# Kernel optimization log

Hardware: AMD Instinct MI355X
Metric: run time of the kernel (lower is better)

## Reference

```python
import jax, jax.numpy as jnp
import numpy as np

# ---- config constants (TwoCompartmentLIFConfig defaults) ----
DT = 1.0                      # ms per Euler step
G_L, E_L = 0.05, 0.0          # somatic leak
G_L_D = 0.03                  # dendritic leak
C_D = 0.5                     # dendritic capacitance
G_C = 0.05                    # soma-dendrite coupling
E_E, E_I = 3.0, -0.5
E_NMDA, E_GABA_B = 3.0, -0.8
E_CA = 4.0
E_ADAPT = -0.5
V_TH, V_RESET, TAU_REF = 1.0, 0.0, 5.0
MG_K, MG_VHALF = 5.0, 0.5     # NMDA Mg2+ block sigmoid
THETA_CA, G_CA_SPIKE = 2.0, 0.3
BAP_AMP = 0.3
ADAPT_INC = 0.0
# conductance decay factors exp(-dt/tau)
D_E  = float(np.exp(-DT / 5.0))
D_I  = float(np.exp(-DT / 10.0))
D_N  = float(np.exp(-DT / 100.0))
D_GB = float(np.exp(-DT / 400.0))
D_CA = float(np.exp(-DT / 20.0))
D_AD = float(np.exp(-DT / 100.0))

T, N = 50, 500000
IN_SCALE = 0.06


def setup_inputs() -> dict:
    key = jax.random.key(0)
    ks = jax.random.split(key, 7)
    names = ["g_exc_basal", "g_inh_basal", "g_nmda_basal", "g_gaba_b_in",
             "g_exc_apical", "g_inh_apical", "g_nmda_apical"]
    return {n: IN_SCALE * jax.random.uniform(k, (T, N), dtype=jnp.float32)
            for n, k in zip(names, ks)}


def _run(g_exc_basal, g_inh_basal, g_nmda_basal, g_gaba_b_in,
         g_exc_apical, g_inh_apical, g_nmda_apical):
    n = g_exc_basal.shape[1]
    z = jnp.zeros((n,), jnp.float32)
    # carry: v_soma, v_dend, gEb, gIb, gNb, gGB, gEa, gIa, gNa, gCa, gAd, ref
    carry0 = (z + E_L, z + E_L, z, z, z, z, z, z, z, z, z, z)

    def step(carry, inp):
        v_s, v_d, gEb, gIb, gNb, gGB, gEa, gIa, gNa, gCa, gAd, ref = carry
        in_Eb, in_Ib, in_Nb, in_GB, in_Ea, in_Ia, in_Na = inp
        # decay + inject synaptic conductances
        gEb = gEb * D_E + in_Eb
        gIb = gIb * D_I + in_Ib
        gNb = gNb * D_N + in_Nb
        gGB = gGB * D_GB + in_GB
        gEa = gEa * D_E + in_Ea
        gIa = gIa * D_I + in_Ia
        gNa = gNa * D_N + in_Na
        gCa = gCa * D_CA
        # NMDA Mg2+ block gated at the LOCAL compartment voltage
        mg_s = jax.nn.sigmoid(MG_K * (v_s - MG_VHALF))
        mg_d = jax.nn.sigmoid(MG_K * (v_d - MG_VHALF))
        # somatic current (C_m = 1)
        I_s = (G_L * (E_L - v_s) + gEb * (E_E - v_s) + gIb * (E_I - v_s)
               + gNb * mg_s * (E_NMDA - v_s) + gGB * (E_GABA_B - v_s)
               + gAd * (E_ADAPT - v_s) + G_C * (v_d - v_s))
        # dendritic current
        I_d = (G_L_D * (E_L - v_d) + gEa * (E_E - v_d) + gIa * (E_I - v_d)
               + gNa * mg_d * (E_NMDA - v_d) + gCa * (E_CA - v_d)
               + G_C * (v_s - v_d))
        refractory = ref > 0.0
        v_s = jnp.where(refractory, V_RESET, v_s + DT * I_s)
        v_d = v_d + (DT / C_D) * I_d
        # spike + reset + refractory
        spike = (v_s >= V_TH) & jnp.logical_not(refractory)
        spike_f = spike.astype(jnp.float32)
        v_s = jnp.where(spike, V_RESET, v_s)
        ref = jnp.where(spike, TAU_REF, jnp.maximum(ref - DT, 0.0))
        gAd = gAd * D_AD + spike_f * ADAPT_INC
        # back-propagating AP depolarises dendrite
        v_d = jnp.where(spike, v_d + BAP_AMP * (E_CA - v_d), v_d)
        # dendritic Ca spike
        gCa = gCa + (v_d >= THETA_CA).astype(jnp.float32) * G_CA_SPIKE
        carry = (v_s, v_d, gEb, gIb, gNb, gGB, gEa, gIa, gNa, gCa, gAd, ref)
        return carry, (spike_f, v_s)

    inputs = (g_exc_basal, g_inh_basal, g_nmda_basal, g_gaba_b_in,
              g_exc_apical, g_inh_apical, g_nmda_apical)
    _, (spikes, v_trace) = jax.lax.scan(step, carry0, inputs)
    return spikes, v_trace  # each [T, N]


def reference(g_exc_basal, g_inh_basal, g_nmda_basal, g_gaba_b_in,
              g_exc_apical, g_inh_apical, g_nmda_apical):
    return _run(g_exc_basal, g_inh_basal, g_nmda_basal, g_gaba_b_in,
                g_exc_apical, g_inh_apical, g_nmda_apical)
```

## Files before the change

kernel.cpp:

```cpp
#include <hip/hip_runtime.h>
#include <math.h>

namespace {
constexpr float D_E   = 0.8187307530779818f;
constexpr float D_I   = 0.9048374180359595f;
constexpr float D_N   = 0.9900498337491681f;
constexpr float D_GB  = 0.9975031223974601f;
constexpr float D_CA  = 0.9512294245007140f;

constexpr float DT      = 1.0f;
constexpr float G_L     = 0.05f;
constexpr float E_L     = 0.0f;
constexpr float G_L_D   = 0.03f;
constexpr float DT_C_D  = 2.0f;
constexpr float G_C     = 0.05f;
constexpr float E_E     = 3.0f;
constexpr float E_I     = -0.5f;
constexpr float E_NMDA  = 3.0f;
constexpr float E_GABA_B= -0.8f;
constexpr float E_CA    = 4.0f;
constexpr float V_TH    = 1.0f;
constexpr float V_RESET = 0.0f;
constexpr float TAU_REF = 5.0f;
constexpr float MG_K    = 5.0f;
constexpr float MG_VHALF= 0.5f;
constexpr float THETA_CA= 2.0f;
constexpr float G_CA_SPIKE = 0.3f;
constexpr float BAP_AMP = 0.3f;
}

__device__ __forceinline__ void lif_step(
    float in_Eb, float in_Ib, float in_Nb, float in_GB,
    float in_Ea, float in_Ia, float in_Na,
    float& v_s, float& v_d,
    float& gEb, float& gIb, float& gNb, float& gGB,
    float& gEa, float& gIa, float& gNa, float& gCa, float& ref,
    float& spike_out, float& v_out)
{
    gEb = gEb * D_E  + in_Eb;
    gIb = gIb * D_I  + in_Ib;
    gNb = gNb * D_N  + in_Nb;
    gGB = gGB * D_GB + in_GB;
    gEa = gEa * D_E  + in_Ea;
    gIa = gIa * D_I  + in_Ia;
    gNa = gNa * D_N  + in_Na;
    gCa = gCa * D_CA;

    const float mg_s = 1.0f / (1.0f + expf(-MG_K * (v_s - MG_VHALF)));
    const float mg_d = 1.0f / (1.0f + expf(-MG_K * (v_d - MG_VHALF)));

    const float I_s = G_L * (E_L - v_s) + gEb * (E_E - v_s) + gIb * (E_I - v_s)
                    + gNb * mg_s * (E_NMDA - v_s) + gGB * (E_GABA_B - v_s)
                    + G_C * (v_d - v_s);
    const float I_d = G_L_D * (E_L - v_d) + gEa * (E_E - v_d) + gIa * (E_I - v_d)
                    + gNa * mg_d * (E_NMDA - v_d) + gCa * (E_CA - v_d)
                    + G_C * (v_s - v_d);

    const bool refractory = ref > 0.0f;
    v_s = refractory ? V_RESET : (v_s + DT * I_s);
    v_d = v_d + DT_C_D * I_d;

    const bool spike = (v_s >= V_TH) && !refractory;
    const float spike_f = spike ? 1.0f : 0.0f;
    v_s = spike ? V_RESET : v_s;
    ref = spike ? TAU_REF : fmaxf(ref - DT, 0.0f);
    v_d = spike ? (v_d + BAP_AMP * (E_CA - v_d)) : v_d;
    gCa = gCa + ((v_d >= THETA_CA) ? G_CA_SPIKE : 0.0f);

    spike_out = spike_f;
    v_out = v_s;
}

__global__ __launch_bounds__(256, 8)
void lif_scalar_pf_kernel(const float* __restrict__ pEb, const float* __restrict__ pIb,
                          const float* __restrict__ pNb, const float* __restrict__ pGB,
                          const float* __restrict__ pEa, const float* __restrict__ pIa,
                          const float* __restrict__ pNa,
                          float* __restrict__ out, int N, int T)
{
    const int i = blockIdx.x * blockDim.x + threadIdx.x;
    if (i >= N) return;

    float v_s = E_L, v_d = E_L;
    float gEb = 0, gIb = 0, gNb = 0, gGB = 0;
    float gEa = 0, gIa = 0, gNa = 0, gCa = 0, ref = 0;

    const size_t vtrace_off = (size_t)T * (size_t)N;

    size_t off = (size_t)i;
    float nEb = pEb[off], nIb = pIb[off], nNb = pNb[off], nGB = pGB[off];
    float nEa = pEa[off], nIa = pIa[off], nNa = pNa[off];

    for (int t = 0; t < T; ++t) {
        const float cEb = nEb, cIb = nIb, cNb = nNb, cGB = nGB;
        const float cEa = nEa, cIa = nIa, cNa = nNa;

        const size_t noff = off + ((t + 1 < T) ? (size_t)N : 0);
        nEb = pEb[noff]; nIb = pIb[noff]; nNb = pNb[noff]; nGB = pGB[noff];
        nEa = pEa[noff]; nIa = pIa[noff]; nNa = pNa[noff];

        float sp, vv;
        lif_step(cEb, cIb, cNb, cGB, cEa, cIa, cNa,
                 v_s, v_d, gEb, gIb, gNb, gGB, gEa, gIa, gNa, gCa, ref,
                 sp, vv);

        out[off]              = sp;
        out[vtrace_off + off] = vv;
        off += (size_t)N;
    }
}

extern "C" void kernel_launch(void* const* d_in, const int* in_sizes, int n_in,
                              void* d_out, int out_size, void* d_ws, size_t ws_size,
                              hipStream_t stream) {
    const float* pEb = (const float*)d_in[0];
    const float* pIb = (const float*)d_in[1];
    const float* pNb = (const float*)d_in[2];
    const float* pGB = (const float*)d_in[3];
    const float* pEa = (const float*)d_in[4];
    const float* pIa = (const float*)d_in[5];
    const float* pNa = (const float*)d_in[6];
    float* out = (float*)d_out;

    const int T = 50;
    const int N = in_sizes[0] / T;

    const int blocks = (N + 255) / 256;
    lif_scalar_pf_kernel<<<blocks, 256, 0, stream>>>(pEb, pIb, pNb, pGB, pEa, pIa, pNa,
                                                     out, N, T);
}
```

Baseline: 180.8 us.

## Process two neurons per thread with float2 loads, two-step prefetch, nontemporal stores

Each thread now handles two adjacent neurons and uses 8-byte vector loads and stores. It keeps two timesteps of inputs in flight as a double-buffered prefetch and writes outputs with nontemporal stores. The sigmoid is switched to fast exp and divide intrinsics, and launch bounds drop to 4 blocks per SM. The goal is more memory-level parallelism and fewer memory instructions in a bandwidth-bound scan, at the cost of more registers, half as many threads, and a small loss of precision in the sigmoid.

```diff
diff --git a/kernel.cpp b/kernel.cpp
--- a/kernel.cpp
+++ b/kernel.cpp
@@ -29,84 +29,151 @@
 constexpr float BAP_AMP = 0.3f;
 }
 
-__device__ __forceinline__ void lif_step(
-    float in_Eb, float in_Ib, float in_Nb, float in_GB,
-    float in_Ea, float in_Ia, float in_Na,
-    float& v_s, float& v_d,
-    float& gEb, float& gIb, float& gNb, float& gGB,
-    float& gEa, float& gIa, float& gNa, float& gCa, float& ref,
-    float& spike_out, float& v_out)
-{
-    gEb = gEb * D_E  + in_Eb;
-    gIb = gIb * D_I  + in_Ib;
-    gNb = gNb * D_N  + in_Nb;
-    gGB = gGB * D_GB + in_GB;
-    gEa = gEa * D_E  + in_Ea;
-    gIa = gIa * D_I  + in_Ia;
-    gNa = gNa * D_N  + in_Na;
-    gCa = gCa * D_CA;
-
-    const float mg_s = 1.0f / (1.0f + expf(-MG_K * (v_s - MG_VHALF)));
-    const float mg_d = 1.0f / (1.0f + expf(-MG_K * (v_d - MG_VHALF)));
-
-    const float I_s = G_L * (E_L - v_s) + gEb * (E_E - v_s) + gIb * (E_I - v_s)
-                    + gNb * mg_s * (E_NMDA - v_s) + gGB * (E_GABA_B - v_s)
-                    + G_C * (v_d - v_s);
-    const float I_d = G_L_D * (E_L - v_d) + gEa * (E_E - v_d) + gIa * (E_I - v_d)
-                    + gNa * mg_d * (E_NMDA - v_d) + gCa * (E_CA - v_d)
-                    + G_C * (v_s - v_d);
-
-    const bool refractory = ref > 0.0f;
-    v_s = refractory ? V_RESET : (v_s + DT * I_s);
-    v_d = v_d + DT_C_D * I_d;
-
-    const bool spike = (v_s >= V_TH) && !refractory;
-    const float spike_f = spike ? 1.0f : 0.0f;
-    v_s = spike ? V_RESET : v_s;
-    ref = spike ? TAU_REF : fmaxf(ref - DT, 0.0f);
-    v_d = spike ? (v_d + BAP_AMP * (E_CA - v_d)) : v_d;
-    gCa = gCa + ((v_d >= THETA_CA) ? G_CA_SPIKE : 0.0f);
-
-    spike_out = spike_f;
-    v_out = v_s;
+typedef float f32x2 __attribute__((ext_vector_type(2)));
+
+__device__ __forceinline__ float fast_sigmoid5(float v) {
+    return __fdividef(1.0f, 1.0f + __expf(-MG_K * (v - MG_VHALF)));
+}
+
+struct State2 {
+    float v_s[2], v_d[2];
+    float gEb[2], gIb[2], gNb[2], gGB[2];
+    float gEa[2], gIa[2], gNa[2], gCa[2], ref[2];
+};
+
+__device__ __forceinline__ void absorb2(
+    const f32x2 iEb, const f32x2 iIb, const f32x2 iNb, const f32x2 iGB,
+    const f32x2 iEa, const f32x2 iIa, const f32x2 iNa, State2& s)
+{
+    s.gEb[0] = s.gEb[0]*D_E  + iEb.x;  s.gEb[1] = s.gEb[1]*D_E  + iEb.y;
+    s.gIb[0] = s.gIb[0]*D_I  + iIb.x;  s.gIb[1] = s.gIb[1]*D_I  + iIb.y;
+    s.gNb[0] = s.gNb[0]*D_N  + iNb.x;  s.gNb[1] = s.gNb[1]*D_N  + iNb.y;
+    s.gGB[0] = s.gGB[0]*D_GB + iGB.x;  s.gGB[1] = s.gGB[1]*D_GB + iGB.y;
+    s.gEa[0] = s.gEa[0]*D_E  + iEa.x;  s.gEa[1] = s.gEa[1]*D_E  + iEa.y;
+    s.gIa[0] = s.gIa[0]*D_I  + iIa.x;  s.gIa[1] = s.gIa[1]*D_I  + iIa.y;
+    s.gNa[0] = s.gNa[0]*D_N  + iNa.x;  s.gNa[1] = s.gNa[1]*D_N  + iNa.y;
+    s.gCa[0] *= D_CA;                  s.gCa[1] *= D_CA;
+}
+
+__device__ __forceinline__ void fire2(State2& s, f32x2& osp, f32x2& ov)
+{
+    #pragma unroll
+    for (int j = 0; j < 2; ++j) {
+        float v_s = s.v_s[j], v_d = s.v_d[j];
+        const float mg_s = fast_sigmoid5(v_s);
+        const float mg_d = fast_sigmoid5(v_d);
+        const float I_s = G_L*(E_L - v_s) + s.gEb[j]*(E_E - v_s) + s.gIb[j]*(E_I - v_s)
+                        + s.gNb[j]*mg_s*(E_NMDA - v_s) + s.gGB[j]*(E_GABA_B - v_s)
+                        + G_C*(v_d - v_s);
+        const float I_d = G_L_D*(E_L - v_d) + s.gEa[j]*(E_E - v_d) + s.gIa[j]*(E_I - v_d)
+                        + s.gNa[j]*mg_d*(E_NMDA - v_d) + s.gCa[j]*(E_CA - v_d)
+                        + G_C*(v_s - v_d);
+        const bool refractory = s.ref[j] > 0.0f;
+        v_s = refractory ? V_RESET : (v_s + DT*I_s);
+        v_d = v_d + DT_C_D*I_d;
+        const bool spike = (v_s >= V_TH) && !refractory;
+        const float spike_f = spike ? 1.0f : 0.0f;
+        v_s = spike ? V_RESET : v_s;
+        s.ref[j] = spike ? TAU_REF : fmaxf(s.ref[j] - DT, 0.0f);
+        v_d = spike ? (v_d + BAP_AMP*(E_CA - v_d)) : v_d;
+        s.gCa[j] += (v_d >= THETA_CA) ? G_CA_SPIKE : 0.0f;
+        s.v_s[j] = v_s; s.v_d[j] = v_d;
+        if (j == 0) { osp.x = spike_f; ov.x = v_s; }
+        else        { osp.y = spike_f; ov.y = v_s; }
+    }
+}
+
+#define LOAD7(S, OFF)                                     \
+    S##Eb = *(const f32x2*)(pEb + (OFF));                 \
+    S##Ib = *(const f32x2*)(pIb + (OFF));                 \
+    S##Nb = *(const f32x2*)(pNb + (OFF));                 \
+    S##GB = *(const f32x2*)(pGB + (OFF));                 \
+    S##Ea = *(const f32x2*)(pEa + (OFF));                 \
+    S##Ia = *(const f32x2*)(pIa + (OFF));                 \
+    S##Na = *(const f32x2*)(pNa + (OFF));
+
+__global__ __launch_bounds__(256, 4)
+void lif_f2_pf2_kernel(const float* __restrict__ pEb, const float* __restrict__ pIb,
+                       const float* __restrict__ pNb, const float* __restrict__ pGB,
+                       const float* __restrict__ pEa, const float* __restrict__ pIa,
+                       const float* __restrict__ pNa,
+                       float* __restrict__ out, int N, int T)
+{
+    const int tid = blockIdx.x * blockDim.x + threadIdx.x;
+    const long long base = (long long)tid * 2;
+    if (base >= N) return;
+
+    State2 s;
+    #pragma unroll
+    for (int j = 0; j < 2; ++j) {
+        s.v_s[j] = E_L; s.v_d[j] = E_L;
+        s.gEb[j] = 0; s.gIb[j] = 0; s.gNb[j] = 0; s.gGB[j] = 0;
+        s.gEa[j] = 0; s.gIa[j] = 0; s.gNa[j] = 0; s.gCa[j] = 0; s.ref[j] = 0;
+    }
+
+    const size_t vtr     = (size_t)T * (size_t)N;
+    const size_t lastoff = (size_t)(T - 1) * (size_t)N + (size_t)base;
+
+    size_t off = (size_t)base;
+    f32x2 aEb, aIb, aNb, aGB, aEa, aIa, aNa;
+    f32x2 bEb, bIb, bNb, bGB, bEa, bIa, bNa;
+    LOAD7(a, off)
+    LOAD7(b, off + (size_t)N)
+
+    for (int t = 0; t < T; t += 2) {
+        f32x2 osp, ov;
+
+        absorb2(aEb, aIb, aNb, aGB, aEa, aIa, aNa, s);
+        {
+            const size_t la = (t + 2 < T) ? off + 2 * (size_t)N : lastoff;
+            LOAD7(a, la)
+        }
+        fire2(s, osp, ov);
+        __builtin_nontemporal_store(osp, reinterpret_cast<f32x2*>(out + off));
+        __builtin_nontemporal_store(ov,  reinterpret_cast<f32x2*>(out + vtr + off));
+        off += (size_t)N;
+
+        absorb2(bEb, bIb, bNb, bGB, bEa, bIa, bNa, s);
+        {
+            const size_t lb = (t + 3 < T) ? off + 2 * (size_t)N : lastoff;
+            LOAD7(b, lb)
+        }
+        fire2(s, osp, ov);
+        __builtin_nontemporal_store(osp, reinterpret_cast<f32x2*>(out + off));
+        __builtin_nontemporal_store(ov,  reinterpret_cast<f32x2*>(out + vtr + off));
+        off += (size_t)N;
+    }
 }
 
 __global__ __launch_bounds__(256, 8)
-void lif_scalar_pf_kernel(const float* __restrict__ pEb, const float* __restrict__ pIb,
-                          const float* __restrict__ pNb, const float* __restrict__ pGB,
-                          const float* __restrict__ pEa, const float* __restrict__ pIa,
-                          const float* __restrict__ pNa,
-                          float* __restrict__ out, int N, int T)
+void lif_scalar_kernel(const float* __restrict__ pEb, const float* __restrict__ pIb,
+                       const float* __restrict__ pNb, const float* __restrict__ pGB,
+                       const float* __restrict__ pEa, const float* __restrict__ pIa,
+                       const float* __restrict__ pNa,
+                       float* __restrict__ out, int N, int T)
 {
     const int i = blockIdx.x * blockDim.x + threadIdx.x;
     if (i >= N) return;
-
-    float v_s = E_L, v_d = E_L;
-    float gEb = 0, gIb = 0, gNb = 0, gGB = 0;
-    float gEa = 0, gIa = 0, gNa = 0, gCa = 0, ref = 0;
-
-    const size_t vtrace_off = (size_t)T * (size_t)N;
-
-    size_t off = (size_t)i;
-    float nEb = pEb[off], nIb = pIb[off], nNb = pNb[off], nGB = pGB[off];
-    float nEa = pEa[off], nIa = pIa[off], nNa = pNa[off];
-
+    State2 s;
+    s.v_s[0] = E_L; s.v_d[0] = E_L;
+    s.gEb[0] = 0; s.gIb[0] = 0; s.gNb[0] = 0; s.gGB[0] = 0;
+    s.gEa[0] = 0; s.gIa[0] = 0; s.gNa[0] = 0; s.gCa[0] = 0; s.ref[0] = 0;
+    s.v_s[1] = E_L; s.v_d[1] = E_L;
+    s.gEb[1] = 0; s.gIb[1] = 0; s.gNb[1] = 0; s.gGB[1] = 0;
+    s.gEa[1] = 0; s.gIa[1] = 0; s.gNa[1] = 0; s.gCa[1] = 0; s.ref[1] = 0;
+
+    const size_t vtr = (size_t)T * (size_t)N;
     for (int t = 0; t < T; ++t) {
-        const float cEb = nEb, cIb = nIb, cNb = nNb, cGB = nGB;
-        const float cEa = nEa, cIa = nIa, cNa = nNa;
-
-        const size_t noff = off + ((t + 1 < T) ? (size_t)N : 0);
-        nEb = pEb[noff]; nIb = pIb[noff]; nNb = pNb[noff]; nGB = pGB[noff];
-        nEa = pEa[noff]; nIa = pIa[noff]; nNa = pNa[noff];
-
-        float sp, vv;
-        lif_step(cEb, cIb, cNb, cGB, cEa, cIa, cNa,
-                 v_s, v_d, gEb, gIb, gNb, gGB, gEa, gIa, gNa, gCa, ref,
-                 sp, vv);
-
-        out[off]              = sp;
-        out[vtrace_off + off] = vv;
-        off += (size_t)N;
+        const size_t off = (size_t)t * (size_t)N + (size_t)i;
+        f32x2 iEb = {pEb[off], 0.0f}, iIb = {pIb[off], 0.0f};
+        f32x2 iNb = {pNb[off], 0.0f}, iGB = {pGB[off], 0.0f};
+        f32x2 iEa = {pEa[off], 0.0f}, iIa = {pIa[off], 0.0f};
+        f32x2 iNa = {pNa[off], 0.0f};
+        absorb2(iEb, iIb, iNb, iGB, iEa, iIa, iNa, s);
+        f32x2 osp, ov;
+        fire2(s, osp, ov);
+        out[off]       = osp.x;
+        out[vtr + off] = ov.x;
     }
 }
 
@@ -125,7 +192,14 @@
     const int T = 50;
     const int N = in_sizes[0] / T;
 
-    const int blocks = (N + 255) / 256;
-    lif_scalar_pf_kernel<<<blocks, 256, 0, stream>>>(pEb, pIb, pNb, pGB, pEa, pIa, pNa,
-                                                     out, N, T);
-}
+    if ((N & 1) == 0 && (T & 1) == 0) {
+        const int threads = N / 2;
+        const int blocks = (threads + 255) / 256;
+        lif_f2_pf2_kernel<<<blocks, 256, 0, stream>>>(pEb, pIb, pNb, pGB, pEa, pIa, pNa,
+                                                      out, N, T);
+    } else {
+        const int blocks = (N + 255) / 256;
+        lif_scalar_kernel<<<blocks, 256, 0, stream>>>(pEb, pIb, pNb, pGB, pEa, pIa, pNa,
+                                                      out, N, T);
+    }
+}
```

New measurement: 174.5 us. -3.5%, faster.
